# Optimization experiments

Measured on AMD Instinct MI355X. Metric: run time of the kernel, lower is better.

The kernel has to match this reference:

```python
import jax, jax.numpy as jnp
import numpy as np

E, D, O, G, H, K = 8, 1024, 1024, 512, 2048, 2
B = 8192

def _xavier(key, shape):
    fan_in, fan_out = shape[-2], shape[-1]
    lim = float(np.sqrt(6.0 / (fan_in + fan_out)))
    return jax.random.uniform(key, shape, jnp.float32, -lim, lim)

def setup_inputs() -> dict:
    key = jax.random.key(0)
    ks = jax.random.split(key, 6)
    x = jax.random.normal(ks[0], (B, D), jnp.float32)
    # stacked expert params (xavier-uniform weights, zero bias like torch init)
    W1 = _xavier(ks[1], (E, D, H))
    b1 = jnp.zeros((E, H), jnp.float32)
    W2 = _xavier(ks[2], (E, H, O))
    b2 = jnp.zeros((E, O), jnp.float32)
    # gate params
    Wg1 = _xavier(ks[3], (D, G))
    bg1 = jnp.zeros((G,), jnp.float32)
    Wg2 = _xavier(ks[4], (G, E))
    bg2 = jnp.zeros((E,), jnp.float32)
    return {"x": x, "W1": W1, "b1": b1, "W2": W2, "b2": b2,
            "Wg1": Wg1, "bg1": bg1, "Wg2": Wg2, "bg2": bg2}

def reference(x, W1, b1, W2, b2, Wg1, bg1, Wg2, bg2):
    batch = x.shape[0]
    # gate (dropout inactive in eval)
    gate_logits = jax.nn.relu(x @ Wg1 + bg1) @ Wg2 + bg2          # [B,E]
    gate_scores = jax.nn.softmax(gate_logits, axis=1)
    top_k_scores, top_k_indices = jax.lax.top_k(gate_scores, K)   # [B,K]
    # dense all-expert MLP (mirrors torch.stack over experts)
    h = jax.nn.relu(jnp.einsum('bd,edh->ebh', x, W1) + b1[:, None, :])   # [E,B,H]
    expert_outputs = jnp.einsum('ebh,eho->beo', h, W2) + b2[None, :, :]  # [B,E,O]
    # gather top-k expert outputs, scale, combine
    selected = jnp.take_along_axis(expert_outputs, top_k_indices[:, :, None], axis=1)  # [B,K,O]
    scaled = selected * top_k_scores[:, :, None]
    scaled = scaled / (jnp.sum(top_k_scores, axis=1, keepdims=True)[:, :, None] + 1e-9)
    combined = jnp.sum(scaled, axis=1)                            # [B,O]
    # auxiliary loss
    one_hot = jax.nn.one_hot(top_k_indices, E, dtype=jnp.float32) # [B,K,E]
    expert_load = jnp.sum(one_hot, axis=(0, 1)) / (batch + 1e-9)
    load_balancing_loss = jnp.var(expert_load, ddof=1)            # torch var is unbiased
    entropy = -jnp.mean(jnp.sum(gate_scores * jnp.log(gate_scores + 1e-9), axis=1))
    aux_loss = load_balancing_loss + entropy
    return combined, aux_loss
```

## Files before the change

### kernel.cpp

```cpp
#include <hip/hip_runtime.h>

#define B_ 8192
#define D_ 1024
#define O_ 1024
#define G_ 512
#define H_ 2048
#define E_ 8
#define ROWSP (B_ * 2 + E_ * 128)
#define TAU 0.01f

typedef unsigned short u16;
using f32x4 = __attribute__((ext_vector_type(4))) float;
using s16x8 = __attribute__((ext_vector_type(8))) short;

__device__ __forceinline__ u16 f2bf(float f) {
  union { float f; unsigned u; } v; v.f = f;
  unsigned r = v.u + 0x7FFFu + ((v.u >> 16) & 1u);
  return (u16)(r >> 16);
}
__device__ __forceinline__ float bf2f(u16 h) {
  union { unsigned u; float f; } v; v.u = ((unsigned)h) << 16; return v.f;
}
__device__ __forceinline__ void gload16(const void* g, void* l) {
  __builtin_amdgcn_global_load_lds(
      (const __attribute__((address_space(1))) unsigned int*)g,
      (__attribute__((address_space(3))) unsigned int*)l, 16, 0, 0);
}
__device__ __forceinline__ int xcd_swz(int bid, int nwg) {
  return (bid & 7) * (nwg >> 3) + (bid >> 3);
}

__global__ __launch_bounds__(256) void k_cast_x(const float* __restrict__ x,
                                                u16* __restrict__ xhi,
                                                u16* __restrict__ xlo) {
  int t = blockIdx.x * 256 + threadIdx.x;
  float4 v = ((const float4*)x)[t];
  u16 h0 = f2bf(v.x), h1 = f2bf(v.y), h2 = f2bf(v.z), h3 = f2bf(v.w);
  ushort4 hi; hi.x = h0; hi.y = h1; hi.z = h2; hi.w = h3;
  ushort4 lo;
  lo.x = f2bf(v.x - bf2f(h0)); lo.y = f2bf(v.y - bf2f(h1));
  lo.z = f2bf(v.z - bf2f(h2)); lo.w = f2bf(v.w - bf2f(h3));
  ((ushort4*)xhi)[t] = hi; ((ushort4*)xlo)[t] = lo;
}

__global__ __launch_bounds__(256) void k_transpose_cast(const float* __restrict__ src,
                                                        u16* __restrict__ dhi,
                                                        u16* __restrict__ dlo,
                                                        int R, int C) {
  __shared__ float tile[32][33];
  size_t bofs = (size_t)blockIdx.z * R * C;
  src += bofs; dhi += bofs; if (dlo) dlo += bofs;
  int tx = threadIdx.x & 31, ty = threadIdx.x >> 5;
  int c0 = blockIdx.x * 32, r0 = blockIdx.y * 32;
#pragma unroll
  for (int p = 0; p < 4; ++p) {
    int r = ty + p * 8;
    tile[r][tx] = src[(size_t)(r0 + r) * C + c0 + tx];
  }
  __syncthreads();
#pragma unroll
  for (int p = 0; p < 4; ++p) {
    int r = ty + p * 8;
    float v = tile[tx][r];
    size_t o = (size_t)(c0 + r) * R + r0 + tx;
    dhi[o] = f2bf(v);
    if (dlo) dlo[o] = f2bf(v - bf2f(f2bf(v)));
  }
}

__global__ __launch_bounds__(256) void k_gate_gemm1(const u16* __restrict__ xhi,
                                                    const u16* __restrict__ xlo,
                                                    const u16* __restrict__ whi,
                                                    const u16* __restrict__ wlo,
                                                    const float* __restrict__ bg1,
                                                    float* __restrict__ G1) {
  __shared__ u16 Ah[128 * 32], Al[128 * 32], Bh[128 * 32], Bl[128 * 32];
  int work = xcd_swz(blockIdx.x, (G_ / 128) * (B_ / 128));
  int m0 = (work >> 2) * 128, n0 = (work & 3) * 128;
  int t = threadIdx.x;
  int wave = t >> 6, lane = t & 63;
  int wm = wave >> 1, wn = wave & 1;

  const f32x4 z = {0.f, 0.f, 0.f, 0.f};
  f32x4 acc[4][4];
#pragma unroll
  for (int i = 0; i < 4; ++i)
#pragma unroll
    for (int j = 0; j < 4; ++j) acc[i][j] = z;

  int ac = (t & 3) * 8;
  for (int k0 = 0; k0 < D_; k0 += 32) {
#pragma unroll
    for (int r = 0; r < 2; ++r) {
      int li = r * 256 + t;
      int row = li >> 2;
      gload16(xhi + (size_t)(m0 + row) * D_ + k0 + ac, &Ah[li * 8]);
      gload16(xlo + (size_t)(m0 + row) * D_ + k0 + ac, &Al[li * 8]);
      gload16(whi + (size_t)(n0 + row) * D_ + k0 + ac, &Bh[li * 8]);
      gload16(wlo + (size_t)(n0 + row) * D_ + k0 + ac, &Bl[li * 8]);
    }
    __syncthreads();
    s16x8 ah[4], al[4], bh[4], bl[4];
#pragma unroll
    for (int i = 0; i < 4; ++i) {
      int ra = (wm * 64 + i * 16 + (lane & 15)) * 32 + (lane >> 4) * 8;
      int rb = (wn * 64 + i * 16 + (lane & 15)) * 32 + (lane >> 4) * 8;
      ah[i] = *(const s16x8*)&Ah[ra]; al[i] = *(const s16x8*)&Al[ra];
      bh[i] = *(const s16x8*)&Bh[rb]; bl[i] = *(const s16x8*)&Bl[rb];
    }
#pragma unroll
    for (int i = 0; i < 4; ++i)
#pragma unroll
      for (int j = 0; j < 4; ++j) {
        acc[i][j] = __builtin_amdgcn_mfma_f32_16x16x32_bf16(ah[i], bh[j], acc[i][j], 0, 0, 0);
        acc[i][j] = __builtin_amdgcn_mfma_f32_16x16x32_bf16(ah[i], bl[j], acc[i][j], 0, 0, 0);
        acc[i][j] = __builtin_amdgcn_mfma_f32_16x16x32_bf16(al[i], bh[j], acc[i][j], 0, 0, 0);
      }
    __syncthreads();
  }
#pragma unroll
  for (int j = 0; j < 4; ++j) {
    int col = n0 + wn * 64 + j * 16 + (lane & 15);
    float bias = bg1[col];
#pragma unroll
    for (int i = 0; i < 4; ++i)
#pragma unroll
      for (int q = 0; q < 4; ++q) {
        int row = m0 + wm * 64 + i * 16 + (lane >> 4) * 4 + q;
        float v = acc[i][j][q] + bias;
        G1[(size_t)row * G_ + col] = v > 0.f ? v : 0.f;
      }
  }
}

__global__ __launch_bounds__(256) void k_gate_logits(const float* __restrict__ G1,
                                                     const float* __restrict__ Wg2,
                                                     const float* __restrict__ bg2,
                                                     float* __restrict__ logits,
                                                     int* __restrict__ flaglist,
                                                     int* __restrict__ nflag) {
  int t = threadIdx.x, wave = t >> 6, lane = t & 63;
  int row = blockIdx.x * 4 + wave;

  float4 g0 = *(const float4*)(G1 + (size_t)row * G_ + lane * 8);
  float4 g1 = *(const float4*)(G1 + (size_t)row * G_ + lane * 8 + 4);
  float g[8] = {g0.x, g0.y, g0.z, g0.w, g1.x, g1.y, g1.z, g1.w};
  float p[8] = {0, 0, 0, 0, 0, 0, 0, 0};
#pragma unroll
  for (int cc = 0; cc < 8; ++cc) {
    int c = lane * 8 + cc;
    float4 w0 = *(const float4*)(Wg2 + c * 8);
    float4 w1 = *(const float4*)(Wg2 + c * 8 + 4);
    p[0] += g[cc] * w0.x; p[1] += g[cc] * w0.y; p[2] += g[cc] * w0.z; p[3] += g[cc] * w0.w;
    p[4] += g[cc] * w1.x; p[5] += g[cc] * w1.y; p[6] += g[cc] * w1.z; p[7] += g[cc] * w1.w;
  }
#pragma unroll
  for (int off = 32; off >= 1; off >>= 1)
#pragma unroll
    for (int e = 0; e < 8; ++e) p[e] += __shfl_xor(p[e], off);
  if (lane == 0) {
    float l1 = -1e30f, l2 = -1e30f, l3 = -1e30f;
#pragma unroll
    for (int e = 0; e < 8; ++e) {
      float v = p[e] + bg2[e];
      logits[(size_t)row * 8 + e] = v;
      if (v > l1) { l3 = l2; l2 = l1; l1 = v; }
      else if (v > l2) { l3 = l2; l2 = v; }
      else if (v > l3) { l3 = v; }
    }
    if (l2 - l3 < TAU) {
      int pos = atomicAdd(nflag, 1);
      flaglist[pos] = row;
    }
  }
}

__global__ __launch_bounds__(256) void k_gate_fixup(const float* __restrict__ x,
                                                    const float* __restrict__ Wg1,
                                                    const float* __restrict__ bg1,
                                                    const float* __restrict__ Wg2,
                                                    const float* __restrict__ bg2,
                                                    const int* __restrict__ flaglist,
                                                    const int* __restrict__ nflag,
                                                    float* __restrict__ logits) {
  __shared__ float xs[1024];
  __shared__ float red[256][9];
  int t = threadIdx.x;
  int n = *nflag;
  for (int i = blockIdx.x; i < n; i += gridDim.x) {
    int row = flaglist[i];
    ((float4*)xs)[t] = ((const float4*)(x + (size_t)row * D_))[t];
    __syncthreads();
    int c0 = t * 2;
    float h0 = 0.f, h1 = 0.f;
#pragma unroll 8
    for (int d = 0; d < D_; ++d) {
      float xv = xs[d];
      float2 w = *(const float2*)(Wg1 + (size_t)d * G_ + c0);
      h0 += xv * w.x; h1 += xv * w.y;
    }
    h0 += bg1[c0]; h1 += bg1[c0 + 1];
    h0 = h0 > 0.f ? h0 : 0.f; h1 = h1 > 0.f ? h1 : 0.f;
#pragma unroll
    for (int e = 0; e < 8; ++e)
      red[t][e] = h0 * Wg2[c0 * 8 + e] + h1 * Wg2[(c0 + 1) * 8 + e];
    __syncthreads();
    for (int s = 128; s >= 1; s >>= 1) {
      if (t < s) {
#pragma unroll
        for (int e = 0; e < 8; ++e) red[t][e] += red[t + s][e];
      }
      __syncthreads();
    }
    if (t < 8) logits[(size_t)row * 8 + t] = red[0][t] + bg2[t];
    __syncthreads();
  }
}

__global__ __launch_bounds__(256) void k_gate_final(const float* __restrict__ logits,
                                                    int* __restrict__ topidx,
                                                    float* __restrict__ wnorm,
                                                    int* __restrict__ counts,
                                                    float* __restrict__ entacc) {
  __shared__ int cnt_s[8];
  __shared__ float ent_s[4];
  int t = threadIdx.x;
  if (t < 8) cnt_s[t] = 0;
  __syncthreads();
  int row = blockIdx.x * 256 + t;
  float4 a = ((const float4*)logits)[(size_t)row * 2];
  float4 b = ((const float4*)logits)[(size_t)row * 2 + 1];
  float L[8] = {a.x, a.y, a.z, a.w, b.x, b.y, b.z, b.w};
  float m = L[0];
#pragma unroll
  for (int e = 1; e < 8; ++e) m = fmaxf(m, L[e]);
  float s[8], Z = 0.f;
#pragma unroll
  for (int e = 0; e < 8; ++e) { s[e] = expf(L[e] - m); Z += s[e]; }
  float inv = 1.f / Z;
  float sc[8];
#pragma unroll
  for (int e = 0; e < 8; ++e) sc[e] = s[e] * inv;
  int i1 = 0;
#pragma unroll
  for (int e = 1; e < 8; ++e) if (L[e] > L[i1]) i1 = e;
  int i2 = (i1 == 0) ? 1 : 0;
#pragma unroll
  for (int e = 0; e < 8; ++e) if (e != i1 && L[e] > L[i2]) i2 = e;
  float s1 = sc[i1], s2 = sc[i2];
  float denom = s1 + s2 + 1e-9f;
  topidx[row * 2] = i1; topidx[row * 2 + 1] = i2;
  wnorm[row * 2] = s1 / denom; wnorm[row * 2 + 1] = s2 / denom;
  atomicAdd(&cnt_s[i1], 1); atomicAdd(&cnt_s[i2], 1);
  float ent = 0.f;
#pragma unroll
  for (int e = 0; e < 8; ++e) ent -= sc[e] * logf(sc[e] + 1e-9f);
#pragma unroll
  for (int off = 32; off >= 1; off >>= 1) ent += __shfl_xor(ent, off);
  if ((t & 63) == 0) ent_s[t >> 6] = ent;
  __syncthreads();
  if (t == 0) atomicAdd(entacc, ent_s[0] + ent_s[1] + ent_s[2] + ent_s[3]);
  if (t < 8) atomicAdd(&counts[t], cnt_s[t]);
}

__global__ void k_scan(const int* __restrict__ counts, const float* __restrict__ entacc,
                       int* __restrict__ aoff, float* __restrict__ aux_out) {
  if (threadIdx.x == 0 && blockIdx.x == 0) {
    int off = 0; aoff[0] = 0;
    float ld[8]; float mean = 0.f;
    for (int e = 0; e < 8; ++e) {
      ld[e] = (float)counts[e] / (8192.0f + 1e-9f);
      mean += ld[e];
      off += ((counts[e] + 127) >> 7) << 7;
      aoff[e + 1] = off;
    }
    mean *= 0.125f;
    float var = 0.f;
    for (int e = 0; e < 8; ++e) { float d = ld[e] - mean; var += d * d; }
    var *= (1.0f / 7.0f);
    *aux_out = var + entacc[0] / 8192.0f;
  }
}

__global__ __launch_bounds__(256) void k_scatter(const int* __restrict__ topidx,
                                                 const float* __restrict__ wnorm,
                                                 const int* __restrict__ aoff,
                                                 int* __restrict__ fill,
                                                 int* __restrict__ tok_list,
                                                 float* __restrict__ wroute,
                                                 int* __restrict__ pos_of) {
  int t = blockIdx.x * 256 + threadIdx.x;
  if (t >= B_ * 2) return;
  int e = topidx[t];
  int pos = aoff[e] + atomicAdd(&fill[e], 1);
  tok_list[pos] = t >> 1;
  wroute[pos] = wnorm[t];
  pos_of[t] = pos;
}

__global__ __launch_bounds__(256) void k_egemm1(const u16* __restrict__ xhi,
                                                const u16* __restrict__ w1t,
                                                const float* __restrict__ b1v,
                                                const int* __restrict__ tok_list,
                                                const int* __restrict__ aoff,
                                                u16* __restrict__ hbuf) {
  __shared__ u16 As[128 * 32], Bs[128 * 32];
  int work = xcd_swz(blockIdx.x, (H_ / 128) * (ROWSP / 128));
  int rt = work >> 4;
  int n0 = (work & 15) * 128;
  int row0 = rt * 128;
  if (row0 >= aoff[8]) return;
  int e = 0;
  while (row0 >= aoff[e + 1]) ++e;
  int t = threadIdx.x, wave = t >> 6, lane = t & 63;
  int wm = wave >> 1, wn = wave & 1;
  const u16* w1e = w1t + (size_t)e * H_ * D_;

  int arow = t >> 2, ac = (t & 3) * 8;
  int tok0 = tok_list[row0 + arow];       if ((unsigned)tok0 >= B_) tok0 = 0;
  int tok1 = tok_list[row0 + 64 + arow];  if ((unsigned)tok1 >= B_) tok1 = 0;
  const u16* a0 = xhi + (size_t)tok0 * D_ + ac;
  const u16* a1 = xhi + (size_t)tok1 * D_ + ac;
  const u16* bb0 = w1e + (size_t)(n0 + arow) * D_ + ac;
  const u16* bb1 = w1e + (size_t)(n0 + 64 + arow) * D_ + ac;

  const f32x4 z = {0.f, 0.f, 0.f, 0.f};
  f32x4 acc[4][4];
#pragma unroll
  for (int i = 0; i < 4; ++i)
#pragma unroll
    for (int j = 0; j < 4; ++j) acc[i][j] = z;

  for (int k0 = 0; k0 < D_; k0 += 32) {
    gload16(a0 + k0, &As[t * 8]);
    gload16(a1 + k0, &As[(256 + t) * 8]);
    gload16(bb0 + k0, &Bs[t * 8]);
    gload16(bb1 + k0, &Bs[(256 + t) * 8]);
    __syncthreads();
    s16x8 af[4], bf[4];
#pragma unroll
    for (int i = 0; i < 4; ++i) {
      af[i] = *(const s16x8*)&As[(wm * 64 + i * 16 + (lane & 15)) * 32 + (lane >> 4) * 8];
      bf[i] = *(const s16x8*)&Bs[(wn * 64 + i * 16 + (lane & 15)) * 32 + (lane >> 4) * 8];
    }
#pragma unroll
    for (int i = 0; i < 4; ++i)
#pragma unroll
      for (int j = 0; j < 4; ++j)
        acc[i][j] = __builtin_amdgcn_mfma_f32_16x16x32_bf16(af[i], bf[j], acc[i][j], 0, 0, 0);
    __syncthreads();
  }
#pragma unroll
  for (int j = 0; j < 4; ++j) {
    int col = n0 + wn * 64 + j * 16 + (lane & 15);
    float bias = b1v[e * H_ + col];
#pragma unroll
    for (int i = 0; i < 4; ++i)
#pragma unroll
      for (int q = 0; q < 4; ++q) {
        int row = row0 + wm * 64 + i * 16 + (lane >> 4) * 4 + q;
        float v = acc[i][j][q] + bias;
        hbuf[(size_t)row * H_ + col] = f2bf(v > 0.f ? v : 0.f);
      }
  }
}

__global__ __launch_bounds__(256) void k_egemm2(const u16* __restrict__ hbuf,
                                                const u16* __restrict__ w2t,
                                                const float* __restrict__ b2v,
                                                const int* __restrict__ aoff,
                                                const float* __restrict__ wroute,
                                                u16* __restrict__ rbuf) {
  __shared__ u16 As[128 * 32], Bs[128 * 32];
  int work = xcd_swz(blockIdx.x, (O_ / 128) * (ROWSP / 128));
  int rt = work >> 3;
  int n0 = (work & 7) * 128;
  int row0 = rt * 128;
  if (row0 >= aoff[8]) return;
  int e = 0;
  while (row0 >= aoff[e + 1]) ++e;
  int t = threadIdx.x, wave = t >> 6, lane = t & 63;
  int wm = wave >> 1, wn = wave & 1;
  const u16* w2e = w2t + (size_t)e * O_ * H_;

  int arow = t >> 2, ac = (t & 3) * 8;
  const u16* a0 = hbuf + (size_t)(row0 + arow) * H_ + ac;
  const u16* a1 = hbuf + (size_t)(row0 + 64 + arow) * H_ + ac;
  const u16* bb0 = w2e + (size_t)(n0 + arow) * H_ + ac;
  const u16* bb1 = w2e + (size_t)(n0 + 64 + arow) * H_ + ac;

  const f32x4 z = {0.f, 0.f, 0.f, 0.f};
  f32x4 acc[4][4];
#pragma unroll
  for (int i = 0; i < 4; ++i)
#pragma unroll
    for (int j = 0; j < 4; ++j) acc[i][j] = z;

  for (int k0 = 0; k0 < H_; k0 += 32) {
    gload16(a0 + k0, &As[t * 8]);
    gload16(a1 + k0, &As[(256 + t) * 8]);
    gload16(bb0 + k0, &Bs[t * 8]);
    gload16(bb1 + k0, &Bs[(256 + t) * 8]);
    __syncthreads();
    s16x8 af[4], bf[4];
#pragma unroll
    for (int i = 0; i < 4; ++i) {
      af[i] = *(const s16x8*)&As[(wm * 64 + i * 16 + (lane & 15)) * 32 + (lane >> 4) * 8];
      bf[i] = *(const s16x8*)&Bs[(wn * 64 + i * 16 + (lane & 15)) * 32 + (lane >> 4) * 8];
    }
#pragma unroll
    for (int i = 0; i < 4; ++i)
#pragma unroll
      for (int j = 0; j < 4; ++j)
        acc[i][j] = __builtin_amdgcn_mfma_f32_16x16x32_bf16(af[i], bf[j], acc[i][j], 0, 0, 0);
    __syncthreads();
  }
#pragma unroll
  for (int i = 0; i < 4; ++i)
#pragma unroll
    for (int q = 0; q < 4; ++q) {
      int row = row0 + wm * 64 + i * 16 + (lane >> 4) * 4 + q;
      float wv = wroute[row];
#pragma unroll
      for (int j = 0; j < 4; ++j) {
        int col = n0 + wn * 64 + j * 16 + (lane & 15);
        float bias = b2v[e * O_ + col];
        rbuf[(size_t)row * O_ + col] = f2bf((acc[i][j][q] + bias) * wv);
      }
    }
}

__global__ __launch_bounds__(256) void k_combine(const u16* __restrict__ rbuf,
                                                 const int* __restrict__ pos_of,
                                                 float* __restrict__ out) {
  int t = threadIdx.x;
  int tok = blockIdx.x * 2 + (t >> 7);
  int c = (t & 127) * 8;
  int p0 = pos_of[tok * 2], p1 = pos_of[tok * 2 + 1];
  const u16* r0 = rbuf + (size_t)p0 * O_ + c;
  const u16* r1 = rbuf + (size_t)p1 * O_ + c;
  ushort4 a0 = *(const ushort4*)r0, a1 = *(const ushort4*)(r0 + 4);
  ushort4 b0 = *(const ushort4*)r1, b1 = *(const ushort4*)(r1 + 4);
  float4 o0, o1;
  o0.x = bf2f(a0.x) + bf2f(b0.x); o0.y = bf2f(a0.y) + bf2f(b0.y);
  o0.z = bf2f(a0.z) + bf2f(b0.z); o0.w = bf2f(a0.w) + bf2f(b0.w);
  o1.x = bf2f(a1.x) + bf2f(b1.x); o1.y = bf2f(a1.y) + bf2f(b1.y);
  o1.z = bf2f(a1.z) + bf2f(b1.z); o1.w = bf2f(a1.w) + bf2f(b1.w);
  float* op = out + (size_t)tok * O_ + c;
  *(float4*)op = o0; *(float4*)(op + 4) = o1;
}

static const size_t o_xhi  = 0;
static const size_t o_xlo  = o_xhi + (size_t)B_ * D_ * 2;
static const size_t o_w1t  = o_xlo + (size_t)B_ * D_ * 2;
static const size_t o_w2t  = o_w1t + (size_t)E_ * H_ * D_ * 2;
static const size_t o_wg1h = o_w2t + (size_t)E_ * O_ * H_ * 2;
static const size_t o_wg1l = o_wg1h + (size_t)G_ * D_ * 2;
static const size_t o_G1   = o_wg1l + (size_t)G_ * D_ * 2;
static const size_t o_h    = o_G1 + (size_t)B_ * G_ * 4;
static const size_t o_idx  = o_h + (size_t)ROWSP * H_ * 2;
static const size_t o_wn   = o_idx + (size_t)B_ * 2 * 4;
static const size_t o_pos  = o_wn + (size_t)B_ * 2 * 4;
static const size_t o_tok  = o_pos + (size_t)B_ * 2 * 4;
static const size_t o_wr   = o_tok + (size_t)ROWSP * 4;
static const size_t o_cnt  = o_wr + (size_t)ROWSP * 4;
static const size_t o_fill = o_cnt + 32;
static const size_t o_ent  = o_cnt + 64;
static const size_t o_nfl  = o_cnt + 96;
static const size_t o_aoff = o_cnt + 128;
static const size_t o_logits = o_cnt + 256;
static const size_t o_flag   = o_logits + (size_t)B_ * 8 * 4;
static const size_t o_rbuf = o_xlo;

extern "C" void kernel_launch(void* const* d_in, const int* in_sizes, int n_in,
                              void* d_out, int out_size, void* d_ws, size_t ws_size,
                              hipStream_t stream) {
  const float* x   = (const float*)d_in[0];
  const float* W1  = (const float*)d_in[1];
  const float* b1  = (const float*)d_in[2];
  const float* W2  = (const float*)d_in[3];
  const float* b2  = (const float*)d_in[4];
  const float* Wg1 = (const float*)d_in[5];
  const float* bg1 = (const float*)d_in[6];
  const float* Wg2 = (const float*)d_in[7];
  const float* bg2 = (const float*)d_in[8];
  float* out = (float*)d_out;
  char* ws = (char*)d_ws;

  u16* xhi  = (u16*)(ws + o_xhi);
  u16* xlo  = (u16*)(ws + o_xlo);
  u16* w1t  = (u16*)(ws + o_w1t);
  u16* w2t  = (u16*)(ws + o_w2t);
  u16* wg1h = (u16*)(ws + o_wg1h);
  u16* wg1l = (u16*)(ws + o_wg1l);
  float* G1 = (float*)(ws + o_G1);
  u16* hbuf = (u16*)(ws + o_h);
  int* topidx = (int*)(ws + o_idx);
  float* wnorm = (float*)(ws + o_wn);
  int* pos_of = (int*)(ws + o_pos);
  int* tok_list = (int*)(ws + o_tok);
  float* wroute = (float*)(ws + o_wr);
  int* counts = (int*)(ws + o_cnt);
  int* fill = (int*)(ws + o_fill);
  float* entacc = (float*)(ws + o_ent);
  int* nflag = (int*)(ws + o_nfl);
  int* aoff = (int*)(ws + o_aoff);
  float* logits = (float*)(ws + o_logits);
  int* flaglist = (int*)(ws + o_flag);
  u16* rbuf = (u16*)(ws + o_rbuf);

  hipMemsetAsync(ws + o_cnt, 0, 128, stream);

  k_cast_x<<<(B_ * D_ / 4) / 256, 256, 0, stream>>>(x, xhi, xlo);
  k_transpose_cast<<<dim3(G_ / 32, D_ / 32, 1), 256, 0, stream>>>(Wg1, wg1h, wg1l, D_, G_);
  k_transpose_cast<<<dim3(H_ / 32, D_ / 32, E_), 256, 0, stream>>>(W1, w1t, nullptr, D_, H_);
  k_transpose_cast<<<dim3(O_ / 32, H_ / 32, E_), 256, 0, stream>>>(W2, w2t, nullptr, H_, O_);

  k_gate_gemm1<<<(G_ / 128) * (B_ / 128), 256, 0, stream>>>(xhi, xlo, wg1h, wg1l, bg1, G1);
  k_gate_logits<<<B_ / 4, 256, 0, stream>>>(G1, Wg2, bg2, logits, flaglist, nflag);
  k_gate_fixup<<<128, 256, 0, stream>>>(x, Wg1, bg1, Wg2, bg2, flaglist, nflag, logits);
  k_gate_final<<<B_ / 256, 256, 0, stream>>>(logits, topidx, wnorm, counts, entacc);
  k_scan<<<1, 64, 0, stream>>>(counts, entacc, aoff, out + (size_t)B_ * O_);
  k_scatter<<<(B_ * 2) / 256, 256, 0, stream>>>(topidx, wnorm, aoff, fill, tok_list, wroute, pos_of);

  k_egemm1<<<(H_ / 128) * (ROWSP / 128), 256, 0, stream>>>(xhi, w1t, b1, tok_list, aoff, hbuf);
  k_egemm2<<<(O_ / 128) * (ROWSP / 128), 256, 0, stream>>>(hbuf, w2t, b2, aoff, wroute, rbuf);
  k_combine<<<B_ / 2, 256, 0, stream>>>(rbuf, pos_of, out);
}
```

Measured before the change: 526.2 us.

## Double-buffer expert GEMM LDS tiles and use k-slab-major shared layout

The shared-memory tile layout becomes k-slab-major: each 8-element k chunk is stored contiguously across 64 rows, which removes bank conflicts on the fragment reads in all three GEMMs. Both expert GEMMs also get double-buffered LDS, so the global-to-LDS loads for the next k step are issued before the MFMAs on the current step. This aims to hide load latency and reduce LDS conflicts, at the cost of twice the shared memory per block, which may lower occupancy. The hunks shown do not include the synchronisation at the end of each loop iteration, so correctness depends on the existing barrier there.

```diff
diff --git a/kernel.cpp b/kernel.cpp
--- a/kernel.cpp
+++ b/kernel.cpp
@@ -28,6 +28,9 @@
 }
 __device__ __forceinline__ int xcd_swz(int bid, int nwg) {
   return (bid & 7) * (nwg >> 3) + (bid >> 3);
+}
+__device__ __forceinline__ int frag_idx(int half, int lane, int i) {
+  return half * 2048 + (lane >> 4) * 512 + (i * 16 + (lane & 15)) * 8;
 }
 
 __global__ __launch_bounds__(256) void k_cast_x(const float* __restrict__ x,
@@ -74,7 +77,7 @@
                                                     const u16* __restrict__ wlo,
                                                     const float* __restrict__ bg1,
                                                     float* __restrict__ G1) {
-  __shared__ u16 Ah[128 * 32], Al[128 * 32], Bh[128 * 32], Bl[128 * 32];
+  __shared__ u16 Ah[4096], Al[4096], Bh[4096], Bl[4096];
   int work = xcd_swz(blockIdx.x, (G_ / 128) * (B_ / 128));
   int m0 = (work >> 2) * 128, n0 = (work & 3) * 128;
   int t = threadIdx.x;
@@ -88,25 +91,29 @@
 #pragma unroll
     for (int j = 0; j < 4; ++j) acc[i][j] = z;
 
-  int ac = (t & 3) * 8;
+  int r6 = t & 63, ks8 = (t >> 6) * 8;
+  const u16* xh0 = xhi + (size_t)(m0 + r6) * D_ + ks8;
+  const u16* xh1 = xhi + (size_t)(m0 + 64 + r6) * D_ + ks8;
+  const u16* xl0 = xlo + (size_t)(m0 + r6) * D_ + ks8;
+  const u16* xl1 = xlo + (size_t)(m0 + 64 + r6) * D_ + ks8;
+  const u16* wh0 = whi + (size_t)(n0 + r6) * D_ + ks8;
+  const u16* wh1 = whi + (size_t)(n0 + 64 + r6) * D_ + ks8;
+  const u16* wl0 = wlo + (size_t)(n0 + r6) * D_ + ks8;
+  const u16* wl1 = wlo + (size_t)(n0 + 64 + r6) * D_ + ks8;
+
   for (int k0 = 0; k0 < D_; k0 += 32) {
-#pragma unroll
-    for (int r = 0; r < 2; ++r) {
-      int li = r * 256 + t;
-      int row = li >> 2;
-      gload16(xhi + (size_t)(m0 + row) * D_ + k0 + ac, &Ah[li * 8]);
-      gload16(xlo + (size_t)(m0 + row) * D_ + k0 + ac, &Al[li * 8]);
-      gload16(whi + (size_t)(n0 + row) * D_ + k0 + ac, &Bh[li * 8]);
-      gload16(wlo + (size_t)(n0 + row) * D_ + k0 + ac, &Bl[li * 8]);
-    }
+    gload16(xh0 + k0, &Ah[t * 8]); gload16(xh1 + k0, &Ah[2048 + t * 8]);
+    gload16(xl0 + k0, &Al[t * 8]); gload16(xl1 + k0, &Al[2048 + t * 8]);
+    gload16(wh0 + k0, &Bh[t * 8]); gload16(wh1 + k0, &Bh[2048 + t * 8]);
+    gload16(wl0 + k0, &Bl[t * 8]); gload16(wl1 + k0, &Bl[2048 + t * 8]);
     __syncthreads();
     s16x8 ah[4], al[4], bh[4], bl[4];
 #pragma unroll
     for (int i = 0; i < 4; ++i) {
-      int ra = (wm * 64 + i * 16 + (lane & 15)) * 32 + (lane >> 4) * 8;
-      int rb = (wn * 64 + i * 16 + (lane & 15)) * 32 + (lane >> 4) * 8;
-      ah[i] = *(const s16x8*)&Ah[ra]; al[i] = *(const s16x8*)&Al[ra];
-      bh[i] = *(const s16x8*)&Bh[rb]; bl[i] = *(const s16x8*)&Bl[rb];
+      ah[i] = *(const s16x8*)&Ah[frag_idx(wm, lane, i)];
+      al[i] = *(const s16x8*)&Al[frag_idx(wm, lane, i)];
+      bh[i] = *(const s16x8*)&Bh[frag_idx(wn, lane, i)];
+      bl[i] = *(const s16x8*)&Bl[frag_idx(wn, lane, i)];
     }
 #pragma unroll
     for (int i = 0; i < 4; ++i)
@@ -304,7 +311,7 @@
                                                 const int* __restrict__ tok_list,
                                                 const int* __restrict__ aoff,
                                                 u16* __restrict__ hbuf) {
-  __shared__ u16 As[128 * 32], Bs[128 * 32];
+  __shared__ u16 As[2][4096], Bs[2][4096];
   int work = xcd_swz(blockIdx.x, (H_ / 128) * (ROWSP / 128));
   int rt = work >> 4;
   int n0 = (work & 15) * 128;
@@ -316,13 +323,13 @@
   int wm = wave >> 1, wn = wave & 1;
   const u16* w1e = w1t + (size_t)e * H_ * D_;
 
-  int arow = t >> 2, ac = (t & 3) * 8;
-  int tok0 = tok_list[row0 + arow];       if ((unsigned)tok0 >= B_) tok0 = 0;
-  int tok1 = tok_list[row0 + 64 + arow];  if ((unsigned)tok1 >= B_) tok1 = 0;
-  const u16* a0 = xhi + (size_t)tok0 * D_ + ac;
-  const u16* a1 = xhi + (size_t)tok1 * D_ + ac;
-  const u16* bb0 = w1e + (size_t)(n0 + arow) * D_ + ac;
-  const u16* bb1 = w1e + (size_t)(n0 + 64 + arow) * D_ + ac;
+  int r6 = t & 63, ks8 = (t >> 6) * 8;
+  int tok0 = tok_list[row0 + r6];       if ((unsigned)tok0 >= B_) tok0 = 0;
+  int tok1 = tok_list[row0 + 64 + r6];  if ((unsigned)tok1 >= B_) tok1 = 0;
+  const u16* a0 = xhi + (size_t)tok0 * D_ + ks8;
+  const u16* a1 = xhi + (size_t)tok1 * D_ + ks8;
+  const u16* bb0 = w1e + (size_t)(n0 + r6) * D_ + ks8;
+  const u16* bb1 = w1e + (size_t)(n0 + 64 + r6) * D_ + ks8;
 
   const f32x4 z = {0.f, 0.f, 0.f, 0.f};
   f32x4 acc[4][4];
@@ -331,17 +338,26 @@
 #pragma unroll
     for (int j = 0; j < 4; ++j) acc[i][j] = z;
 
-  for (int k0 = 0; k0 < D_; k0 += 32) {
-    gload16(a0 + k0, &As[t * 8]);
-    gload16(a1 + k0, &As[(256 + t) * 8]);
-    gload16(bb0 + k0, &Bs[t * 8]);
-    gload16(bb1 + k0, &Bs[(256 + t) * 8]);
-    __syncthreads();
+  gload16(a0, &As[0][t * 8]);  gload16(a1, &As[0][2048 + t * 8]);
+  gload16(bb0, &Bs[0][t * 8]); gload16(bb1, &Bs[0][2048 + t * 8]);
+  __syncthreads();
+
+  const int NT = D_ / 32;
+  for (int kt = 0; kt < NT; ++kt) {
+    const u16* Sa = As[kt & 1];
+    const u16* Sb = Bs[kt & 1];
+    if (kt + 1 < NT) {
+      int k1 = (kt + 1) * 32;
+      u16* Da = As[(kt + 1) & 1];
+      u16* Db = Bs[(kt + 1) & 1];
+      gload16(a0 + k1, &Da[t * 8]);  gload16(a1 + k1, &Da[2048 + t * 8]);
+      gload16(bb0 + k1, &Db[t * 8]); gload16(bb1 + k1, &Db[2048 + t * 8]);
+    }
     s16x8 af[4], bf[4];
 #pragma unroll
     for (int i = 0; i < 4; ++i) {
-      af[i] = *(const s16x8*)&As[(wm * 64 + i * 16 + (lane & 15)) * 32 + (lane >> 4) * 8];
-      bf[i] = *(const s16x8*)&Bs[(wn * 64 + i * 16 + (lane & 15)) * 32 + (lane >> 4) * 8];
+      af[i] = *(const s16x8*)&Sa[frag_idx(wm, lane, i)];
+      bf[i] = *(const s16x8*)&Sb[frag_idx(wn, lane, i)];
     }
 #pragma unroll
     for (int i = 0; i < 4; ++i)
@@ -371,7 +387,7 @@
                                                 const int* __restrict__ aoff,
                                                 const float* __restrict__ wroute,
                                                 u16* __restrict__ rbuf) {
-  __shared__ u16 As[128 * 32], Bs[128 * 32];
+  __shared__ u16 As[2][4096], Bs[2][4096];
   int work = xcd_swz(blockIdx.x, (O_ / 128) * (ROWSP / 128));
   int rt = work >> 3;
   int n0 = (work & 7) * 128;
@@ -383,11 +399,11 @@
   int wm = wave >> 1, wn = wave & 1;
   const u16* w2e = w2t + (size_t)e * O_ * H_;
 
-  int arow = t >> 2, ac = (t & 3) * 8;
-  const u16* a0 = hbuf + (size_t)(row0 + arow) * H_ + ac;
-  const u16* a1 = hbuf + (size_t)(row0 + 64 + arow) * H_ + ac;
-  const u16* bb0 = w2e + (size_t)(n0 + arow) * H_ + ac;
-  const u16* bb1 = w2e + (size_t)(n0 + 64 + arow) * H_ + ac;
+  int r6 = t & 63, ks8 = (t >> 6) * 8;
+  const u16* a0 = hbuf + (size_t)(row0 + r6) * H_ + ks8;
+  const u16* a1 = hbuf + (size_t)(row0 + 64 + r6) * H_ + ks8;
+  const u16* bb0 = w2e + (size_t)(n0 + r6) * H_ + ks8;
+  const u16* bb1 = w2e + (size_t)(n0 + 64 + r6) * H_ + ks8;
 
   const f32x4 z = {0.f, 0.f, 0.f, 0.f};
   f32x4 acc[4][4];
@@ -396,17 +412,26 @@
 #pragma unroll
     for (int j = 0; j < 4; ++j) acc[i][j] = z;
 
-  for (int k0 = 0; k0 < H_; k0 += 32) {
-    gload16(a0 + k0, &As[t * 8]);
-    gload16(a1 + k0, &As[(256 + t) * 8]);
-    gload16(bb0 + k0, &Bs[t * 8]);
-    gload16(bb1 + k0, &Bs[(256 + t) * 8]);
-    __syncthreads();
+  gload16(a0, &As[0][t * 8]);  gload16(a1, &As[0][2048 + t * 8]);
+  gload16(bb0, &Bs[0][t * 8]); gload16(bb1, &Bs[0][2048 + t * 8]);
+  __syncthreads();
+
+  const int NT = H_ / 32;
+  for (int kt = 0; kt < NT; ++kt) {
+    const u16* Sa = As[kt & 1];
+    const u16* Sb = Bs[kt & 1];
+    if (kt + 1 < NT) {
+      int k1 = (kt + 1) * 32;
+      u16* Da = As[(kt + 1) & 1];
+      u16* Db = Bs[(kt + 1) & 1];
+      gload16(a0 + k1, &Da[t * 8]);  gload16(a1 + k1, &Da[2048 + t * 8]);
+      gload16(bb0 + k1, &Db[t * 8]); gload16(bb1 + k1, &Db[2048 + t * 8]);
+    }
     s16x8 af[4], bf[4];
 #pragma unroll
     for (int i = 0; i < 4; ++i) {
-      af[i] = *(const s16x8*)&As[(wm * 64 + i * 16 + (lane & 15)) * 32 + (lane >> 4) * 8];
-      bf[i] = *(const s16x8*)&Bs[(wn * 64 + i * 16 + (lane & 15)) * 32 + (lane >> 4) * 8];
+      af[i] = *(const s16x8*)&Sa[frag_idx(wm, lane, i)];
+      bf[i] = *(const s16x8*)&Sb[frag_idx(wn, lane, i)];
     }
 #pragma unroll
     for (int i = 0; i < 4; ++i)
```

Measured after the change: 627.5 us. +19.3%, slower.
